# Optimization experiments

Hardware: AMD Instinct MI355X
Metric: run time of the kernel (lower is better)

## Reference

```python
import jax, jax.numpy as jnp
import numpy as np

B, L, H = 2, 2048, 2048
NH, KVH = 16, 4
D = H // NH          # 128
G = NH // KVH        # 4 query heads per kv head
LN_EPS = 1e-12


def setup_inputs() -> dict:
    key = jax.random.key(0)
    ks = jax.random.split(key, 6)
    s = 0.02
    return {
        "hidden_state": jax.random.normal(ks[0], (B, L, H), jnp.float32),
        "mask": jnp.zeros((B, 1, 1, L), jnp.float32),
        "Wq": jax.random.normal(ks[1], (H, H), jnp.float32) * s,
        "bq": jnp.zeros((H,), jnp.float32),
        "Wk": jax.random.normal(ks[2], (KVH * D, H), jnp.float32) * s,
        "bk": jnp.zeros((KVH * D,), jnp.float32),
        "Wv": jax.random.normal(ks[3], (KVH * D, H), jnp.float32) * s,
        "bv": jnp.zeros((KVH * D,), jnp.float32),
        "Wo": jax.random.normal(ks[4], (H, H), jnp.float32) * s,
        "bo": jnp.zeros((H,), jnp.float32),
        "ln_g": jnp.ones((H,), jnp.float32),
        "ln_b": jnp.zeros((H,), jnp.float32),
    }


def _layernorm(x, g, b):
    mu = jnp.mean(x, axis=-1, keepdims=True)
    var = jnp.mean(jnp.square(x - mu), axis=-1, keepdims=True)
    return (x - mu) * jax.lax.rsqrt(var + LN_EPS) * g + b


def reference(hidden_state, mask, Wq, bq, Wk, bk, Wv, bv, Wo, bo, ln_g, ln_b):
    x = hidden_state
    # projections: b l (h d)
    q = x @ Wq.T + bq            # [B,L,NH*D]
    k = x @ Wk.T + bk            # [B,L,KVH*D]
    v = x @ Wv.T + bv            # [B,L,KVH*D]
    # b l (h d) -> b h l d, with q heads grouped per kv head (GQA broadcast,
    # mathematically identical to repeat_kv + dense SDPA)
    q = q.reshape(B, L, KVH, G, D).transpose(0, 2, 3, 1, 4)   # [B,KVH,G,L,D]
    k = k.reshape(B, L, KVH, D).transpose(0, 2, 1, 3)         # [B,KVH,L,D]
    v = v.reshape(B, L, KVH, D).transpose(0, 2, 1, 3)         # [B,KVH,L,D]
    scale = 1.0 / jnp.sqrt(jnp.float32(D))
    scores = jnp.einsum('bkgld,bkmd->bkglm', q, k) * scale    # [B,KVH,G,L,L]
    scores = scores + mask[:, :, None]                         # broadcast [B,1,1,1,L]
    attn = jax.nn.softmax(scores, axis=-1)
    out = jnp.einsum('bkglm,bkmd->bkgld', attn, v)            # [B,KVH,G,L,D]
    out = out.transpose(0, 3, 1, 2, 4).reshape(B, L, H)       # b h l d -> b l (h d)
    # SelfOutput: dense + residual + layernorm
    out = out @ Wo.T + bo
    return _layernorm(out + x, ln_g, ln_b)
```

## Files before the change

### kernel.cpp

```cpp
#include <hip/hip_runtime.h>
#include <math.h>

typedef short v8s __attribute__((ext_vector_type(8)));
typedef float v4f __attribute__((ext_vector_type(4)));
typedef unsigned long long ull;

constexpr int L_ = 2048;
constexpr int H_ = 2048;
constexpr float LOG2E = 1.4426950408889634f;
constexpr float QSCALE = 0.08838834764831845f * LOG2E;

__device__ inline unsigned short f2bf(float f) {
    unsigned int u = __float_as_uint(f);
    u += 0x7fffu + ((u >> 16) & 1u);
    return (unsigned short)(u >> 16);
}

__device__ inline unsigned int pk2bf(float lo, float hi) {
    unsigned int a = __float_as_uint(lo) + 0x8000u;
    unsigned int b = __float_as_uint(hi) + 0x8000u;
    return __builtin_amdgcn_perm(b, a, 0x07060302);
}

__device__ inline void async16(const void* g, void* l) {
    __builtin_amdgcn_global_load_lds(
        (const __attribute__((address_space(1))) unsigned int*)g,
        (__attribute__((address_space(3))) unsigned int*)l, 16, 0, 0);
}

__global__ __launch_bounds__(256) void conv_all(
    const float* __restrict__ x,  const float* __restrict__ wq,
    const float* __restrict__ wk, const float* __restrict__ wv,
    const float* __restrict__ wo, const float* __restrict__ mask,
    unsigned short* __restrict__ xb, unsigned short* __restrict__ wqkvb,
    unsigned short* __restrict__ wob, float* __restrict__ maskL)
{
    int u = blockIdx.x * 256 + threadIdx.x;
    const float* s;
    unsigned short* d;
    if (u < 1048576)      { s = x  + (size_t)u * 8;             d = xb   + (size_t)u * 8; }
    else if (u < 1572864) { size_t t = (size_t)(u - 1048576) * 8; s = wq + t; d = wqkvb + t; }
    else if (u < 1703936) { size_t t = (size_t)(u - 1572864) * 8; s = wk + t; d = wqkvb + (size_t)2048 * 2048 + t; }
    else if (u < 1835008) { size_t t = (size_t)(u - 1703936) * 8; s = wv + t; d = wqkvb + (size_t)2560 * 2048 + t; }
    else if (u < 2359296) { size_t t = (size_t)(u - 1835008) * 8; s = wo + t; d = wob + t; }
    else if (u < 2359808) {
        int m = (u - 2359296) * 8;
        float4 a = *(const float4*)(mask + m);
        float4 b = *(const float4*)(mask + m + 4);
        float4 oa = {a.x * LOG2E, a.y * LOG2E, a.z * LOG2E, a.w * LOG2E};
        float4 ob = {b.x * LOG2E, b.y * LOG2E, b.z * LOG2E, b.w * LOG2E};
        *(float4*)(maskL + m) = oa;
        *(float4*)(maskL + m + 4) = ob;
        return;
    } else return;
    float4 a = *(const float4*)s;
    float4 b = *(const float4*)(s + 4);
    v8s o;
    o[0] = (short)f2bf(a.x); o[1] = (short)f2bf(a.y);
    o[2] = (short)f2bf(a.z); o[3] = (short)f2bf(a.w);
    o[4] = (short)f2bf(b.x); o[5] = (short)f2bf(b.y);
    o[6] = (short)f2bf(b.z); o[7] = (short)f2bf(b.w);
    *(v8s*)d = o;
}

template <int MODE>
__global__ __launch_bounds__(256) void gemm_mfma(
    const unsigned short* __restrict__ A, const unsigned short* __restrict__ W,
    const float* __restrict__ b0, const float* __restrict__ b1,
    const float* __restrict__ b2,
    unsigned short* __restrict__ oq, unsigned short* __restrict__ ok,
    unsigned short* __restrict__ ov,
    float* __restrict__ of, const float* __restrict__ resid,
    int K, int N)
{
    __shared__ short SM[3 * 8192];

    const int tid  = threadIdx.x;
    const int lane = tid & 63;
    const int wave = tid >> 6;
    const int lid  = lane & 15;
    const int g    = lane >> 4;
    const int wr   = wave >> 1, wc = wave & 1;
    const int row0 = blockIdx.y * 128, col0 = blockIdx.x * 128;

    auto stage = [&](int k0, int buf) {
#pragma unroll
        for (int i = 0; i < 2; ++i) {
            int idx = tid + i * 256;
            int r = idx >> 2, s = idx & 3;
            int c = s ^ ((r >> 1) & 3);
            async16(A + (size_t)(row0 + r) * K + k0 + c * 8,
                    &SM[buf * 8192 + idx * 8]);
            async16(W + (size_t)(col0 + r) * K + k0 + c * 8,
                    &SM[buf * 8192 + 4096 + idx * 8]);
        }
    };

    v4f acc[4][4];
#pragma unroll
    for (int i = 0; i < 4; ++i)
#pragma unroll
        for (int j = 0; j < 4; ++j) acc[i][j] = (v4f){0.f, 0.f, 0.f, 0.f};

    stage(0, 0);
    stage(32, 1);
    int p = 0;
    for (int k0 = 0; k0 < K; k0 += 32) {
        __syncthreads();
        if (k0 + 64 < K) {
            int nb = p + 2; if (nb >= 3) nb -= 3;
            stage(k0 + 64, nb);
        }
        const short* As = &SM[p * 8192];
        const short* Bs = &SM[p * 8192 + 4096];

        v8s af[4], bf[4];
#pragma unroll
        for (int t = 0; t < 4; ++t) {
            int ra = wr * 64 + t * 16 + lid;
            int rb = wc * 64 + t * 16 + lid;
            af[t] = *(const v8s*)&As[ra * 32 + ((g ^ ((ra >> 1) & 3)) * 8)];
            bf[t] = *(const v8s*)&Bs[rb * 32 + ((g ^ ((rb >> 1) & 3)) * 8)];
        }
#pragma unroll
        for (int mt = 0; mt < 4; ++mt)
#pragma unroll
            for (int nt = 0; nt < 4; ++nt)
                acc[mt][nt] = __builtin_amdgcn_mfma_f32_16x16x32_bf16(
                    af[mt], bf[nt], acc[mt][nt], 0, 0, 0);
        if (++p == 3) p = 0;
    }

    const int crow = row0 + wr * 64, ccol = col0 + wc * 64;
    if (MODE == 0) {
#pragma unroll
        for (int mt = 0; mt < 4; ++mt)
#pragma unroll
            for (int nt = 0; nt < 4; ++nt) {
                int cc = ccol + nt * 16 + lid;
                float bb = b0[cc];
#pragma unroll
                for (int r = 0; r < 4; ++r) {
                    int rr = crow + mt * 16 + g * 4 + r;
                    of[(size_t)rr * N + cc] =
                        acc[mt][nt][r] + bb + resid[(size_t)rr * N + cc];
                }
            }
    } else {
        const int seg = (col0 < 2048) ? 0 : (col0 < 2560 ? 1 : 2);
#pragma unroll
        for (int mt = 0; mt < 4; ++mt)
#pragma unroll
            for (int nt = 0; nt < 4; ++nt) {
                int cc = ccol + nt * 16 + lid;
                if (seg == 0) {
                    float bb = b0[cc];
#pragma unroll
                    for (int r = 0; r < 4; ++r) {
                        int rr = crow + mt * 16 + g * 4 + r;
                        oq[(size_t)rr * 2048 + cc] =
                            f2bf((acc[mt][nt][r] + bb) * QSCALE);
                    }
                } else if (seg == 1) {
                    float bb = b1[cc - 2048];
#pragma unroll
                    for (int r = 0; r < 4; ++r) {
                        int rr = crow + mt * 16 + g * 4 + r;
                        ok[(size_t)rr * 512 + (cc - 2048)] =
                            f2bf(acc[mt][nt][r] + bb);
                    }
                } else {
                    float bb = b2[cc - 2560];
#pragma unroll
                    for (int r = 0; r < 4; ++r) {
                        int rr = crow + mt * 16 + g * 4 + r;
                        ov[(size_t)rr * 512 + (cc - 2560)] =
                            f2bf(acc[mt][nt][r] + bb);
                    }
                }
            }
    }
}

__global__ __launch_bounds__(256) void transpose_v(
    const unsigned short* __restrict__ V, unsigned short* __restrict__ Vt)
{
    __shared__ unsigned short T[64][72];
    const int r0 = blockIdx.y * 64;
    const int c0 = blockIdx.x * 64;
    const int tid = threadIdx.x;
    const int r = tid >> 3, c8 = (tid & 7) * 8;
#pragma unroll
    for (int h = 0; h < 2; ++h) {
        v8s val = *(const v8s*)&V[(size_t)(r0 + h * 32 + r) * 512 + c0 + c8];
#pragma unroll
        for (int e = 0; e < 8; ++e) T[c8 + e][h * 32 + r] = (unsigned short)val[e];
    }
    __syncthreads();
#pragma unroll
    for (int h = 0; h < 2; ++h) {
        int idx = tid + h * 256;
        int ci = idx >> 3, ch = (idx & 7) * 8;
        v8s o = *(const v8s*)&T[ci][ch];
        int rr = r0 + ch;
        *(v8s*)&Vt[((size_t)((rr >> 11) * 512 + c0 + ci)) * 2048 + (rr & 2047)] = o;
    }
}

__global__ __launch_bounds__(512) void flash_mfma(
    const unsigned short* __restrict__ Q,
    const unsigned short* __restrict__ K,
    const unsigned short* __restrict__ Vt,
    const float* __restrict__ maskL,
    unsigned short* __restrict__ AO)
{
    __shared__ short K_s[2][32 * 128];
    __shared__ short V_s[2][128 * 32];
    __shared__ short P_s[256 * 32];

    const int tid  = threadIdx.x;
    const int lane = tid & 63;
    const int wave = tid >> 6;
    const int lid  = lane & 15;
    const int g    = lane >> 4;
    const int lh   = (lid >> 2) & 3;
    const int h    = blockIdx.y;
    const int b    = blockIdx.z;
    const int kvh  = h >> 2;
    const int q0   = blockIdx.x * 256;
    const int wq   = wave * 32;

    const unsigned short* pK;
    const unsigned short* pV;
    {
        int kr = tid >> 4, ks = tid & 15;
        pK = K + ((size_t)(b * L_ + kr)) * 512 + kvh * 128 +
             ((ks ^ (kr & 15)) * 8);
        int vd = tid >> 2, vs = tid & 3;
        pV = Vt + ((size_t)(b * 512 + kvh * 128 + vd)) * 2048 +
             ((vs ^ ((vd >> 2) & 3)) * 8);
    }
    short* ldsK0 = &K_s[0][tid * 8];
    short* ldsK1 = &K_s[1][tid * 8];
    short* ldsV0 = &V_s[0][tid * 8];
    short* ldsV1 = &V_s[1][tid * 8];

    v8s bq[2][4];
    {
        const size_t base = ((size_t)(b * L_ + q0 + wq + lid)) * 2048 + h * 128;
#pragma unroll
        for (int qt = 0; qt < 2; ++qt)
#pragma unroll
            for (int kc = 0; kc < 4; ++kc)
                bq[qt][kc] = *(const v8s*)(Q + base + (size_t)qt * 16 * 2048 +
                                           kc * 32 + g * 8);
    }

    v4f oacc[2][8];
#pragma unroll
    for (int mt = 0; mt < 2; ++mt)
#pragma unroll
        for (int nt = 0; nt < 8; ++nt) oacc[mt][nt] = (v4f){0.f, 0.f, 0.f, 0.f};
    float lsm[2] = {0.f, 0.f};

    async16(pK, ldsK0);
    async16(pV, ldsV0);

    for (int it = 0; it < 64; ++it) {
        const int p = it & 1;
        const int k0 = it * 32;
        __syncthreads();
        pK += 32 * 512;
        pV += 32;
        if (it + 1 < 64) {
            async16(pK, p ? ldsK0 : ldsK1);
            async16(pV, p ? ldsV0 : ldsV1);
        }
        const short* Ks = K_s[p];
        const short* Vs = V_s[p];

        v4f sacc[2][2];
#pragma unroll
        for (int kt = 0; kt < 2; ++kt) {
            float4 mk = *(const float4*)&maskL[b * L_ + k0 + kt * 16 + g * 4];
            v4f seed = {mk.x, mk.y, mk.z, mk.w};
            sacc[kt][0] = seed;
            sacc[kt][1] = seed;
        }
#pragma unroll
        for (int kc = 0; kc < 4; ++kc)
#pragma unroll
            for (int kt = 0; kt < 2; ++kt) {
                v8s ak = *(const v8s*)&Ks[(kt * 16 + lid) * 128 +
                                          (((kc * 4 + g) ^ lid) * 8)];
#pragma unroll
                for (int qt = 0; qt < 2; ++qt)
                    sacc[kt][qt] = __builtin_amdgcn_mfma_f32_16x16x32_bf16(
                        ak, bq[qt][kc], sacc[kt][qt], 0, 0, 0);
            }

#pragma unroll
        for (int kt = 0; kt < 2; ++kt)
#pragma unroll
            for (int qt = 0; qt < 2; ++qt) {
                float e0 = __builtin_amdgcn_exp2f(sacc[kt][qt][0]);
                float e1 = __builtin_amdgcn_exp2f(sacc[kt][qt][1]);
                float e2 = __builtin_amdgcn_exp2f(sacc[kt][qt][2]);
                float e3 = __builtin_amdgcn_exp2f(sacc[kt][qt][3]);
                lsm[qt] += (e0 + e1) + (e2 + e3);
                uint2 pk;
                pk.x = pk2bf(e0, e1);
                pk.y = pk2bf(e2, e3);
                int qrow = wq + qt * 16 + lid;
                int slot = (kt * 2 + (g >> 1)) ^ lh;
                *(uint2*)&P_s[qrow * 32 + slot * 8 + (g & 1) * 4] = pk;
            }

        v8s ap[2];
#pragma unroll
        for (int mt = 0; mt < 2; ++mt)
            ap[mt] = *(const v8s*)&P_s[(wq + mt * 16 + lid) * 32 +
                                       ((g ^ lh) * 8)];
#pragma unroll
        for (int nt = 0; nt < 8; ++nt) {
            v8s bv = *(const v8s*)&Vs[(nt * 16 + lid) * 32 + ((g ^ lh) * 8)];
#pragma unroll
            for (int mt = 0; mt < 2; ++mt)
                oacc[mt][nt] = __builtin_amdgcn_mfma_f32_16x16x32_bf16(
                    ap[mt], bv, oacc[mt][nt], 0, 0, 0);
        }
    }

#pragma unroll
    for (int qt = 0; qt < 2; ++qt) {
        lsm[qt] += __shfl_xor(lsm[qt], 16);
        lsm[qt] += __shfl_xor(lsm[qt], 32);
    }
#pragma unroll
    for (int mt = 0; mt < 2; ++mt) {
        float linv[4];
#pragma unroll
        for (int r = 0; r < 4; ++r) linv[r] = 1.0f / __shfl(lsm[mt], g * 4 + r);
#pragma unroll
        for (int nt = 0; nt < 8; ++nt)
#pragma unroll
            for (int r = 0; r < 4; ++r) {
                size_t orow = (size_t)(b * L_ + q0 + wq + mt * 16 + g * 4 + r);
                AO[orow * 2048 + h * 128 + nt * 16 + lid] =
                    f2bf(oacc[mt][nt][r] * linv[r]);
            }
    }
}

__global__ __launch_bounds__(256) void ln_kernel(
    const float* __restrict__ P, const float* __restrict__ g,
    const float* __restrict__ bta, float* __restrict__ Out)
{
    const int row = blockIdx.x;
    const int tid = threadIdx.x;
    const float* p = P + (size_t)row * H_;

    float vals[8];
    float s = 0.f;
#pragma unroll
    for (int it = 0; it < 2; ++it) {
        int c = tid * 4 + it * 1024;
        float4 a = *(const float4*)&p[c];
        vals[it * 4 + 0] = a.x; vals[it * 4 + 1] = a.y;
        vals[it * 4 + 2] = a.z; vals[it * 4 + 3] = a.w;
        s += a.x + a.y + a.z + a.w;
    }
    __shared__ float red[4];
    float t = s;
#pragma unroll
    for (int off = 32; off > 0; off >>= 1) t += __shfl_xor(t, off);
    if ((tid & 63) == 0) red[tid >> 6] = t;
    __syncthreads();
    float mean = (red[0] + red[1] + red[2] + red[3]) * (1.f / (float)H_);

    float vsum = 0.f;
#pragma unroll
    for (int i = 0; i < 8; ++i) {
        float d = vals[i] - mean;
        vsum += d * d;
    }
    __syncthreads();
    t = vsum;
#pragma unroll
    for (int off = 32; off > 0; off >>= 1) t += __shfl_xor(t, off);
    if ((tid & 63) == 0) red[tid >> 6] = t;
    __syncthreads();
    float var = (red[0] + red[1] + red[2] + red[3]) * (1.f / (float)H_);
    float rs  = 1.f / sqrtf(var + 1e-12f);

#pragma unroll
    for (int it = 0; it < 2; ++it) {
        int c = tid * 4 + it * 1024;
        float4 gv = *(const float4*)&g[c];
        float4 bv = *(const float4*)&bta[c];
        float4 ov;
        ov.x = (vals[it * 4 + 0] - mean) * rs * gv.x + bv.x;
        ov.y = (vals[it * 4 + 1] - mean) * rs * gv.y + bv.y;
        ov.z = (vals[it * 4 + 2] - mean) * rs * gv.z + bv.z;
        ov.w = (vals[it * 4 + 3] - mean) * rs * gv.w + bv.w;
        *(float4*)&Out[(size_t)row * H_ + c] = ov;
    }
}

extern "C" void kernel_launch(void* const* d_in, const int* in_sizes, int n_in,
                              void* d_out, int out_size, void* d_ws, size_t ws_size,
                              hipStream_t stream)
{
    const float* x    = (const float*)d_in[0];
    const float* mask = (const float*)d_in[1];
    const float* Wq   = (const float*)d_in[2];
    const float* bq   = (const float*)d_in[3];
    const float* Wk   = (const float*)d_in[4];
    const float* bk   = (const float*)d_in[5];
    const float* Wv   = (const float*)d_in[6];
    const float* bv   = (const float*)d_in[7];
    const float* Wo   = (const float*)d_in[8];
    const float* bo   = (const float*)d_in[9];
    const float* lng  = (const float*)d_in[10];
    const float* lnb  = (const float*)d_in[11];
    float* out = (float*)d_out;

    char* ws = (char*)d_ws;
    unsigned short* xb    = (unsigned short*)(ws);
    unsigned short* wqkv  = (unsigned short*)(ws + 16777216);
    float*          maskL = (float*)         (ws + 29360128);
    unsigned short* q     = (unsigned short*)(ws + 29376512);
    unsigned short* k     = (unsigned short*)(ws + 46153728);
    unsigned short* vnat  = (unsigned short*)(ws + 50348032);
    unsigned short* vt    = (unsigned short*)(ws + 54542336);
    unsigned short* ao    = (unsigned short*)(ws + 58736640);
    unsigned short* wob   = (unsigned short*)(ws + 75513856);
    float*          pj    = (float*)(ws);

    dim3 blk(256);
    conv_all<<<9218, blk, 0, stream>>>(x, Wq, Wk, Wv, Wo, mask,
                                       xb, wqkv, wob, maskL);

    gemm_mfma<3><<<dim3(24, 32), blk, 0, stream>>>(
        xb, wqkv, bq, bk, bv, q, k, vnat, nullptr, nullptr, 2048, 3072);

    transpose_v<<<dim3(8, 64), blk, 0, stream>>>(vnat, vt);

    flash_mfma<<<dim3(8, 16, 2), dim3(512), 0, stream>>>(q, k, vt, maskL, ao);

    gemm_mfma<0><<<dim3(16, 32), blk, 0, stream>>>(
        ao, wob, bo, nullptr, nullptr, nullptr, nullptr, nullptr, pj, x, 2048, 2048);
    ln_kernel<<<4096, blk, 0, stream>>>(pj, lng, lnb, out);
}
```

Baseline: 344.9 us.

## Keep softmax probabilities in registers and halve flash block size

Measured after the change: 356.2 us. 1.03x slower.

```diff
diff --git a/kernel.cpp b/kernel.cpp
--- a/kernel.cpp
+++ b/kernel.cpp
@@ -2,6 +2,7 @@
 #include <math.h>
 
 typedef short v8s __attribute__((ext_vector_type(8)));
+typedef short v4s __attribute__((ext_vector_type(4)));
 typedef float v4f __attribute__((ext_vector_type(4)));
 typedef unsigned long long ull;
 
@@ -207,7 +208,7 @@
     }
 }
 
-__global__ __launch_bounds__(512) void flash_mfma(
+__global__ __launch_bounds__(256) void flash_mfma(
     const unsigned short* __restrict__ Q,
     const unsigned short* __restrict__ K,
     const unsigned short* __restrict__ Vt,
@@ -216,18 +217,16 @@
 {
     __shared__ short K_s[2][32 * 128];
     __shared__ short V_s[2][128 * 32];
-    __shared__ short P_s[256 * 32];
 
     const int tid  = threadIdx.x;
     const int lane = tid & 63;
     const int wave = tid >> 6;
     const int lid  = lane & 15;
     const int g    = lane >> 4;
-    const int lh   = (lid >> 2) & 3;
     const int h    = blockIdx.y;
     const int b    = blockIdx.z;
     const int kvh  = h >> 2;
-    const int q0   = blockIdx.x * 256;
+    const int q0   = blockIdx.x * 128;
     const int wq   = wave * 32;
 
     const unsigned short* pK;
@@ -238,12 +237,8 @@
              ((ks ^ (kr & 15)) * 8);
         int vd = tid >> 2, vs = tid & 3;
         pV = Vt + ((size_t)(b * 512 + kvh * 128 + vd)) * 2048 +
-             ((vs ^ ((vd >> 2) & 3)) * 8);
-    }
-    short* ldsK0 = &K_s[0][tid * 8];
-    short* ldsK1 = &K_s[1][tid * 8];
-    short* ldsV0 = &V_s[0][tid * 8];
-    short* ldsV1 = &V_s[1][tid * 8];
+             ((vs ^ ((vd >> 1) & 3)) * 8);
+    }
 
     v8s bq[2][4];
     {
@@ -263,8 +258,10 @@
         for (int nt = 0; nt < 8; ++nt) oacc[mt][nt] = (v4f){0.f, 0.f, 0.f, 0.f};
     float lsm[2] = {0.f, 0.f};
 
-    async16(pK, ldsK0);
-    async16(pV, ldsV0);
+    async16(pK,              &K_s[0][tid * 8]);
+    async16(pK + 16 * 512,   &K_s[0][(tid + 256) * 8]);
+    async16(pV,              &V_s[0][tid * 8]);
+    async16(pV + 64 * 2048,  &V_s[0][(tid + 256) * 8]);
 
     for (int it = 0; it < 64; ++it) {
         const int p = it & 1;
@@ -273,8 +270,12 @@
         pK += 32 * 512;
         pV += 32;
         if (it + 1 < 64) {
-            async16(pK, p ? ldsK0 : ldsK1);
-            async16(pV, p ? ldsV0 : ldsV1);
+            short* dK = K_s[p ^ 1];
+            short* dV = V_s[p ^ 1];
+            async16(pK,              &dK[tid * 8]);
+            async16(pK + 16 * 512,   &dK[(tid + 256) * 8]);
+            async16(pV,              &dV[tid * 8]);
+            async16(pV + 64 * 2048,  &dV[(tid + 256) * 8]);
         }
         const short* Ks = K_s[p];
         const short* Vs = V_s[p];
@@ -299,35 +300,38 @@
                         ak, bq[qt][kc], sacc[kt][qt], 0, 0, 0);
             }
 
-#pragma unroll
-        for (int kt = 0; kt < 2; ++kt)
-#pragma unroll
-            for (int qt = 0; qt < 2; ++qt) {
-                float e0 = __builtin_amdgcn_exp2f(sacc[kt][qt][0]);
-                float e1 = __builtin_amdgcn_exp2f(sacc[kt][qt][1]);
-                float e2 = __builtin_amdgcn_exp2f(sacc[kt][qt][2]);
-                float e3 = __builtin_amdgcn_exp2f(sacc[kt][qt][3]);
-                lsm[qt] += (e0 + e1) + (e2 + e3);
-                uint2 pk;
-                pk.x = pk2bf(e0, e1);
-                pk.y = pk2bf(e2, e3);
-                int qrow = wq + qt * 16 + lid;
-                int slot = (kt * 2 + (g >> 1)) ^ lh;
-                *(uint2*)&P_s[qrow * 32 + slot * 8 + (g & 1) * 4] = pk;
-            }
-
         v8s ap[2];
 #pragma unroll
-        for (int mt = 0; mt < 2; ++mt)
-            ap[mt] = *(const v8s*)&P_s[(wq + mt * 16 + lid) * 32 +
-                                       ((g ^ lh) * 8)];
+        for (int qt = 0; qt < 2; ++qt) {
+            float e0 = __builtin_amdgcn_exp2f(sacc[0][qt][0]);
+            float e1 = __builtin_amdgcn_exp2f(sacc[0][qt][1]);
+            float e2 = __builtin_amdgcn_exp2f(sacc[0][qt][2]);
+            float e3 = __builtin_amdgcn_exp2f(sacc[0][qt][3]);
+            float f0 = __builtin_amdgcn_exp2f(sacc[1][qt][0]);
+            float f1 = __builtin_amdgcn_exp2f(sacc[1][qt][1]);
+            float f2 = __builtin_amdgcn_exp2f(sacc[1][qt][2]);
+            float f3 = __builtin_amdgcn_exp2f(sacc[1][qt][3]);
+            lsm[qt] += ((e0 + e1) + (e2 + e3)) + ((f0 + f1) + (f2 + f3));
+            union { uint4 u; v8s v; } pa;
+            pa.u.x = pk2bf(e0, e1);
+            pa.u.y = pk2bf(e2, e3);
+            pa.u.z = pk2bf(f0, f1);
+            pa.u.w = pk2bf(f2, f3);
+            ap[qt] = pa.v;
+        }
+
 #pragma unroll
         for (int nt = 0; nt < 8; ++nt) {
-            v8s bv = *(const v8s*)&Vs[(nt * 16 + lid) * 32 + ((g ^ lh) * 8)];
+            const int dcol = nt * 16 + lid;
+            const short* vrow = &Vs[dcol * 32];
+            const int fsw = ((dcol >> 1) & 3) << 1;
+            v4s vlo = *(const v4s*)&vrow[(g ^ fsw) * 4];
+            v4s vhi = *(const v4s*)&vrow[((4 | g) ^ fsw) * 4];
+            v8s bvf = __builtin_shufflevector(vlo, vhi, 0, 1, 2, 3, 4, 5, 6, 7);
 #pragma unroll
             for (int mt = 0; mt < 2; ++mt)
                 oacc[mt][nt] = __builtin_amdgcn_mfma_f32_16x16x32_bf16(
-                    ap[mt], bv, oacc[mt][nt], 0, 0, 0);
+                    ap[mt], bvf, oacc[mt][nt], 0, 0, 0);
         }
     }
 
@@ -446,7 +450,7 @@
 
     transpose_v<<<dim3(8, 64), blk, 0, stream>>>(vnat, vt);
 
-    flash_mfma<<<dim3(8, 16, 2), dim3(512), 0, stream>>>(q, k, vt, maskL, ao);
+    flash_mfma<<<dim3(16, 16, 2), dim3(256), 0, stream>>>(q, k, vt, maskL, ao);
 
     gemm_mfma<0><<<dim3(16, 32), blk, 0, stream>>>(
         ao, wob, bo, nullptr, nullptr, nullptr, nullptr, nullptr, pj, x, 2048, 2048);
```
